# Optimization experiments

Measured on AMD Instinct MI355X. Metric: run time of the kernel, lower is better.

The kernel has to match this reference:

```python
import jax, jax.numpy as jnp
import numpy as np

DIM = 512
NUM_HEADS = 8
HEAD_DIM = DIM // NUM_HEADS
EPS = 1e-12  # F.normalize eps


def _l2norm(x):
    # F.normalize(x, dim=-1): x / max(||x||, eps)
    n = jnp.sqrt(jnp.sum(x * x, axis=-1, keepdims=True))
    return x / jnp.maximum(n, EPS)


def setup_inputs() -> dict:
    key = jax.random.key(0)
    ks = jax.random.split(key, 5)
    B, T, D = 4, 2048, DIM
    z = jax.random.normal(ks[0], (B, T, D), dtype=jnp.float32)
    t = jnp.zeros((1,), dtype=jnp.float32)  # unused ODE time
    omega = jax.random.normal(ks[1], (1, 1, D), dtype=jnp.float32) * 0.1
    # nn.Linear default init scale ~ U(-1/sqrt(fan_in), 1/sqrt(fan_in))
    s = 1.0 / np.sqrt(D)
    W_qk = jax.random.uniform(ks[2], (2 * D, D), jnp.float32, -s, s)
    W_out = jax.random.uniform(ks[3], (D, D), jnp.float32, -s, s)
    b_out = jax.random.uniform(ks[4], (D,), jnp.float32, -s, s)
    return {"t": t, "z": z, "omega": omega, "W_qk": W_qk, "W_out": W_out, "b_out": b_out}


def reference(t, z, omega, W_qk, W_out, b_out):
    B, T, D = z.shape
    H, hd = NUM_HEADS, HEAD_DIM
    qk = z @ W_qk.T                      # [B,T,2D]
    q, k = qk[..., :D], qk[..., D:]
    q = _l2norm(q.reshape(B, T, H, hd))  # [B,T,H,hd]
    k = _l2norm(k.reshape(B, T, H, hd))
    # coupling: [B,H,T,T]
    coupling = jnp.einsum("bqhd,bkhd->bhqk", q, k)
    interaction = jnp.sin(coupling)
    force = jnp.einsum("bhqk,bkhd->bqhd", interaction, k).reshape(B, T, D)
    return omega + force @ W_out.T + b_out
```

## Files before the change

### kernel.cpp

```cpp
#include <hip/hip_runtime.h>
#include <hip/hip_bf16.h>

typedef unsigned short u16;
typedef __attribute__((ext_vector_type(8))) short short8;
typedef __attribute__((ext_vector_type(4))) short short4_;
typedef __attribute__((ext_vector_type(4))) float f32x4;

#define B_ 4
#define T_ 2048
#define D_ 512
#define H_ 8
#define M_ (B_*T_)
#define INV2PI 0.15915494309189535f

__device__ u16   g_qb[M_*D_];
__device__ u16   g_kb[M_*D_];
__device__ u16   g_kTp[(size_t)B_*H_*64*T_];
__device__ float g_fA[(size_t)M_*D_];
__device__ float g_fB[(size_t)M_*D_];

__device__ inline u16 f2bf(float f) {
  union { __hip_bfloat16 h; u16 u; } cv;
  cv.h = __float2bfloat16(f);
  return cv.u;
}

__device__ inline float sin2pi(float x) {
#if __has_builtin(__builtin_amdgcn_sinf)
  return __builtin_amdgcn_sinf(x);
#else
  return __sinf(x * 6.283185307179586f);
#endif
}

__device__ inline short8 cvt8(f32x4 a, f32x4 b) {
  short8 o;
  o[0]=(short)f2bf(a[0]); o[1]=(short)f2bf(a[1]); o[2]=(short)f2bf(a[2]); o[3]=(short)f2bf(a[3]);
  o[4]=(short)f2bf(b[0]); o[5]=(short)f2bf(b[1]); o[6]=(short)f2bf(b[2]); o[7]=(short)f2bf(b[3]);
  return o;
}

__device__ inline int perm5(int p) {
  int lg = p >> 3, e = p & 7;
  return (e < 4) ? lg*4 + e : 16 + lg*4 + (e & 3);
}

template<int MODE>
__global__ __launch_bounds__(256, 2)
void gemm_bt(float* __restrict__ Cout, const float* __restrict__ add1,
             const float* __restrict__ add2, const float* __restrict__ Afp,
             const float* __restrict__ Bfp) {
  constexpr int K = 512;
  constexpr int N = (MODE == 0) ? 1024 : 512;
  __shared__ u16 As[128*72];
  __shared__ u16 Bs[128*72];
  const int m0 = blockIdx.x*128, n0 = blockIdx.y*128;
  const int t = threadIdx.x;
  const int w = t>>6, l = t&63;
  const int wr = (w>>1)*64, wc = (w&1)*64;
  const int lg = l>>4, li = l&15;
  const int srow = t>>3, scol = (t&7)*8;

  f32x4 acc[4][4] = {};

  for (int k0 = 0; k0 < K; k0 += 64) {
#pragma unroll
    for (int p = 0; p < 4; ++p) {
      int r = srow + p*32;
      {
        f32x4 b0 = *(const f32x4*)&Bfp[(size_t)(n0+r)*K + k0 + scol];
        f32x4 b1 = *(const f32x4*)&Bfp[(size_t)(n0+r)*K + k0 + scol + 4];
        *(short8*)&Bs[r*72 + scol] = cvt8(b0, b1);
      }
      if (MODE == 0) {
        f32x4 a0 = *(const f32x4*)&Afp[(size_t)(m0+r)*K + k0 + scol];
        f32x4 a1 = *(const f32x4*)&Afp[(size_t)(m0+r)*K + k0 + scol + 4];
        *(short8*)&As[r*72 + scol] = cvt8(a0, a1);
      } else {
        size_t off = (size_t)(m0+r)*K + k0 + scol;
        f32x4 a0 = *(const f32x4*)&g_fA[off];
        f32x4 a1 = *(const f32x4*)&g_fA[off+4];
        f32x4 c0 = *(const f32x4*)&g_fB[off];
        f32x4 c1 = *(const f32x4*)&g_fB[off+4];
        a0 += c0; a1 += c1;
        *(short8*)&As[r*72 + scol] = cvt8(a0, a1);
      }
    }
    __syncthreads();
#pragma unroll
    for (int ks = 0; ks < 2; ++ks) {
      short8 af[4], bf[4];
#pragma unroll
      for (int i = 0; i < 4; ++i)
        af[i] = *(const short8*)&As[(wr + i*16 + li)*72 + ks*32 + lg*8];
#pragma unroll
      for (int j = 0; j < 4; ++j)
        bf[j] = *(const short8*)&Bs[(wc + j*16 + li)*72 + ks*32 + lg*8];
#pragma unroll
      for (int i = 0; i < 4; ++i)
#pragma unroll
        for (int j = 0; j < 4; ++j)
          acc[i][j] = __builtin_amdgcn_mfma_f32_16x16x32_bf16(af[i], bf[j], acc[i][j], 0, 0, 0);
    }
    __syncthreads();
  }

  if (MODE == 0) {
    const bool isq = (n0 < 512);
    u16* dst = isq ? g_qb : g_kb;
    const float qs = isq ? INV2PI : 1.0f;
    const int nb = (isq ? n0 : n0 - 512) + wc;
#pragma unroll
    for (int i = 0; i < 4; ++i) {
#pragma unroll
      for (int r = 0; r < 4; ++r) {
        float s = 0.f;
#pragma unroll
        for (int j = 0; j < 4; ++j) s += acc[i][j][r]*acc[i][j][r];
#pragma unroll
        for (int off = 1; off < 16; off <<= 1) s += __shfl_xor(s, off);
        float sc = qs / fmaxf(sqrtf(s), 1e-12f);
        int row = m0 + wr + i*16 + lg*4 + r;
#pragma unroll
        for (int j = 0; j < 4; ++j)
          dst[(size_t)row*D_ + nb + j*16 + li] = f2bf(acc[i][j][r]*sc);
      }
    }
  } else {
#pragma unroll
    for (int i = 0; i < 4; ++i) {
#pragma unroll
      for (int j = 0; j < 4; ++j) {
        int col = n0 + wc + j*16 + li;
        float badd = add1[col] + add2[col];
#pragma unroll
        for (int r = 0; r < 4; ++r) {
          int row = m0 + wr + i*16 + lg*4 + r;
          Cout[(size_t)row*N + col] = acc[i][j][r] + badd;
        }
      }
    }
  }
}

__global__ void transpose_k_kernel() {
  __shared__ u16 tile[64*72];
  const int t0 = blockIdx.x*64, bh = blockIdx.y;
  const int b = bh>>3, h = bh&7;
  const int t = threadIdx.x;
  {
    int r = t>>2, cs = (t&3)*16;
    const u16* src = g_kb + (size_t)(b*T_ + t0 + r)*D_ + h*64 + cs;
    *(short8*)&tile[r*72 + cs]     = *(const short8*)(src);
    *(short8*)&tile[r*72 + cs + 8] = *(const short8*)(src + 8);
  }
  __syncthreads();
  {
    int d = t>>2, ts = (t&3)*16;
    short8 o0, o1;
#pragma unroll
    for (int j = 0; j < 8; ++j) {
      int p0 = ts + j, p1 = ts + 8 + j;
      int s0 = (p0 & ~31) | perm5(p0 & 31);
      int s1 = (p1 & ~31) | perm5(p1 & 31);
      o0[j] = (short)tile[s0*72 + d];
      o1[j] = (short)tile[s1*72 + d];
    }
    u16* dst = g_kTp + ((size_t)bh*64 + d)*T_ + t0 + ts;
    *(short8*)(dst)     = o0;
    *(short8*)(dst + 8) = o1;
  }
}

__global__ __launch_bounds__(256, 2)
void kuramoto_attn_kernel() {
  __shared__ u16 Ks[2][128*72];
  __shared__ u16 KTs[2][64*136];
  const int wg  = blockIdx.x;
  const int wgp = (wg & 7)*64 + (wg >> 3);
  const int bh = wgp >> 4, qt = (wgp & 15) >> 1, kh = wgp & 1;
  const int b = bh >> 3, h = bh & 7;
  const int t = threadIdx.x;
  const int w = t>>6, l = t&63;
  const int lg = l>>4, li = l&15;

  short8 bq[2][4];
#pragma unroll
  for (int ks = 0; ks < 2; ++ks)
#pragma unroll
    for (int j = 0; j < 4; ++j)
      bq[ks][j] = *(const short8*)&g_qb[(size_t)(b*T_ + qt*256 + w*64 + j*16 + li)*D_
                                        + h*64 + ks*32 + lg*8];

  const int sr = t>>3, sc = (t&7)*8;
  const int sd = t>>4, sk = (t&15)*8;
  const u16* kbase = g_kb  + (size_t)b*T_*D_ + h*64;
  const u16* tbase = g_kTp + (size_t)bh*64*T_;
  const int kt0 = kh*8;

  f32x4 acc_o[4][4] = {};

#pragma unroll
  for (int p = 0; p < 4; ++p) {
    *(short8*)&Ks[0][(sr + p*32)*72 + sc] =
      *(const short8*)&kbase[(size_t)(kt0*128 + sr + p*32)*D_ + sc];
    *(short8*)&KTs[0][(sd + p*16)*136 + sk] =
      *(const short8*)&tbase[(size_t)(sd + p*16)*T_ + kt0*128 + sk];
  }
  __syncthreads();

#pragma unroll 2
  for (int ii = 0; ii < 8; ++ii) {
    const int buf = ii & 1;
    short8 rk[4], rt[4];
    if (ii < 7) {
      const int ktn = kt0 + ii + 1;
#pragma unroll
      for (int p = 0; p < 4; ++p) {
        rk[p] = *(const short8*)&kbase[(size_t)(ktn*128 + sr + p*32)*D_ + sc];
        rt[p] = *(const short8*)&tbase[(size_t)(sd + p*16)*T_ + ktn*128 + sk];
      }
    }

#pragma unroll
    for (int kkp = 0; kkp < 4; ++kkp) {
      f32x4 sacc[2][4] = {};
#pragma unroll
      for (int ks = 0; ks < 2; ++ks) {
        short8 af0 = *(const short8*)&Ks[buf][((2*kkp  )*16 + li)*72 + ks*32 + lg*8];
        short8 af1 = *(const short8*)&Ks[buf][((2*kkp+1)*16 + li)*72 + ks*32 + lg*8];
#pragma unroll
        for (int j = 0; j < 4; ++j) {
          sacc[0][j] = __builtin_amdgcn_mfma_f32_16x16x32_bf16(af0, bq[ks][j], sacc[0][j], 0,0,0);
          sacc[1][j] = __builtin_amdgcn_mfma_f32_16x16x32_bf16(af1, bq[ks][j], sacc[1][j], 0,0,0);
        }
      }
      short8 apv[4];
#pragma unroll
      for (int j = 0; j < 4; ++j) {
        union { unsigned int u[4]; short8 s; } cv;
        cv.u[0] = (unsigned)f2bf(sin2pi(sacc[0][j][0])) | ((unsigned)f2bf(sin2pi(sacc[0][j][1]))<<16);
        cv.u[1] = (unsigned)f2bf(sin2pi(sacc[0][j][2])) | ((unsigned)f2bf(sin2pi(sacc[0][j][3]))<<16);
        cv.u[2] = (unsigned)f2bf(sin2pi(sacc[1][j][0])) | ((unsigned)f2bf(sin2pi(sacc[1][j][1]))<<16);
        cv.u[3] = (unsigned)f2bf(sin2pi(sacc[1][j][2])) | ((unsigned)f2bf(sin2pi(sacc[1][j][3]))<<16);
        apv[j] = cv.s;
      }
#pragma unroll
      for (int di = 0; di < 4; ++di) {
        short8 bv = *(const short8*)&KTs[buf][(di*16 + li)*136 + kkp*32 + lg*8];
#pragma unroll
        for (int j = 0; j < 4; ++j)
          acc_o[j][di] = __builtin_amdgcn_mfma_f32_16x16x32_bf16(apv[j], bv, acc_o[j][di], 0,0,0);
      }
    }

    if (ii < 7) {
#pragma unroll
      for (int p = 0; p < 4; ++p) {
        *(short8*)&Ks[buf^1][(sr + p*32)*72 + sc] = rk[p];
        *(short8*)&KTs[buf^1][(sd + p*16)*136 + sk] = rt[p];
      }
    }
    __syncthreads();
  }

  float* F = kh ? g_fB : g_fA;
#pragma unroll
  for (int j = 0; j < 4; ++j)
#pragma unroll
    for (int di = 0; di < 4; ++di)
#pragma unroll
      for (int r = 0; r < 4; ++r) {
        int row = b*T_ + qt*256 + w*64 + j*16 + lg*4 + r;
        int col = h*64 + di*16 + li;
        F[(size_t)row*D_ + col] = acc_o[j][di][r];
      }
}

extern "C" void kernel_launch(void* const* d_in, const int* in_sizes, int n_in,
                              void* d_out, int out_size, void* d_ws, size_t ws_size,
                              hipStream_t stream) {
  const float* z     = (const float*)d_in[1];
  const float* omega = (const float*)d_in[2];
  const float* Wqk   = (const float*)d_in[3];
  const float* Wout  = (const float*)d_in[4];
  const float* bout  = (const float*)d_in[5];
  float* out = (float*)d_out;

  gemm_bt<0><<<dim3(M_/128, 1024/128), 256, 0, stream>>>(nullptr, nullptr, nullptr, z, Wqk);
  transpose_k_kernel<<<dim3(T_/64, B_*H_), 256, 0, stream>>>();
  kuramoto_attn_kernel<<<512, 256, 0, stream>>>();
  gemm_bt<1><<<dim3(M_/128, 512/128), 256, 0, stream>>>(out, omega, bout, nullptr, Wout);
}
```

Before: 160.1 us.

## Switch to fp16 MFMA, drop key-split partials, software-pipeline QK and sin-PV

All matrix operands move from bf16 to fp16 with packed round-toward-zero conversions. The attention kernel no longer splits keys across two workgroups, so it launches 256 blocks that each loop over all 16 key tiles and write one fp16 force buffer. That buffer is read directly by the output GEMM, which removes the two fp32 partial buffers and their summation. The QK MFMAs for the next sub-tile are interleaved with the sin and PV stage of the previous one to overlap transcendental work with matrix work. This halves the grid to 256 blocks on a GPU with more compute units than that, which risks leaving some units idle, and the pipelining raises register pressure.

```diff
diff --git a/kernel.cpp b/kernel.cpp
--- a/kernel.cpp
+++ b/kernel.cpp
@@ -2,8 +2,10 @@
 #include <hip/hip_bf16.h>
 
 typedef unsigned short u16;
+typedef _Float16 f16;
+typedef __attribute__((ext_vector_type(8))) _Float16 f16x8;
+typedef __attribute__((ext_vector_type(2))) __fp16 h16x2;
 typedef __attribute__((ext_vector_type(8))) short short8;
-typedef __attribute__((ext_vector_type(4))) short short4_;
 typedef __attribute__((ext_vector_type(4))) float f32x4;
 
 #define B_ 4
@@ -13,17 +15,10 @@
 #define M_ (B_*T_)
 #define INV2PI 0.15915494309189535f
 
-__device__ u16   g_qb[M_*D_];
-__device__ u16   g_kb[M_*D_];
-__device__ u16   g_kTp[(size_t)B_*H_*64*T_];
-__device__ float g_fA[(size_t)M_*D_];
-__device__ float g_fB[(size_t)M_*D_];
-
-__device__ inline u16 f2bf(float f) {
-  union { __hip_bfloat16 h; u16 u; } cv;
-  cv.h = __float2bfloat16(f);
-  return cv.u;
-}
+__device__ f16 g_qb[M_*D_];
+__device__ f16 g_kb[M_*D_];
+__device__ f16 g_kTp[(size_t)B_*H_*64*T_];
+__device__ f16 g_force[(size_t)M_*D_];
 
 __device__ inline float sin2pi(float x) {
 #if __has_builtin(__builtin_amdgcn_sinf)
@@ -33,11 +28,13 @@
 #endif
 }
 
-__device__ inline short8 cvt8(f32x4 a, f32x4 b) {
-  short8 o;
-  o[0]=(short)f2bf(a[0]); o[1]=(short)f2bf(a[1]); o[2]=(short)f2bf(a[2]); o[3]=(short)f2bf(a[3]);
-  o[4]=(short)f2bf(b[0]); o[5]=(short)f2bf(b[1]); o[6]=(short)f2bf(b[2]); o[7]=(short)f2bf(b[3]);
-  return o;
+__device__ inline f16x8 cvt8h(f32x4 a, f32x4 b) {
+  union { h16x2 h[4]; f16x8 v; } u;
+  u.h[0] = __builtin_amdgcn_cvt_pkrtz(a[0], a[1]);
+  u.h[1] = __builtin_amdgcn_cvt_pkrtz(a[2], a[3]);
+  u.h[2] = __builtin_amdgcn_cvt_pkrtz(b[0], b[1]);
+  u.h[3] = __builtin_amdgcn_cvt_pkrtz(b[2], b[3]);
+  return u.v;
 }
 
 __device__ inline int perm5(int p) {
@@ -52,8 +49,8 @@
              const float* __restrict__ Bfp) {
   constexpr int K = 512;
   constexpr int N = (MODE == 0) ? 1024 : 512;
-  __shared__ u16 As[128*72];
-  __shared__ u16 Bs[128*72];
+  __shared__ f16 As[128*72];
+  __shared__ f16 Bs[128*72];
   const int m0 = blockIdx.x*128, n0 = blockIdx.y*128;
   const int t = threadIdx.x;
   const int w = t>>6, l = t&63;
@@ -70,44 +67,39 @@
       {
         f32x4 b0 = *(const f32x4*)&Bfp[(size_t)(n0+r)*K + k0 + scol];
         f32x4 b1 = *(const f32x4*)&Bfp[(size_t)(n0+r)*K + k0 + scol + 4];
-        *(short8*)&Bs[r*72 + scol] = cvt8(b0, b1);
+        *(f16x8*)&Bs[r*72 + scol] = cvt8h(b0, b1);
       }
       if (MODE == 0) {
         f32x4 a0 = *(const f32x4*)&Afp[(size_t)(m0+r)*K + k0 + scol];
         f32x4 a1 = *(const f32x4*)&Afp[(size_t)(m0+r)*K + k0 + scol + 4];
-        *(short8*)&As[r*72 + scol] = cvt8(a0, a1);
+        *(f16x8*)&As[r*72 + scol] = cvt8h(a0, a1);
       } else {
-        size_t off = (size_t)(m0+r)*K + k0 + scol;
-        f32x4 a0 = *(const f32x4*)&g_fA[off];
-        f32x4 a1 = *(const f32x4*)&g_fA[off+4];
-        f32x4 c0 = *(const f32x4*)&g_fB[off];
-        f32x4 c1 = *(const f32x4*)&g_fB[off+4];
-        a0 += c0; a1 += c1;
-        *(short8*)&As[r*72 + scol] = cvt8(a0, a1);
+        *(short8*)&As[r*72 + scol] =
+          *(const short8*)&g_force[(size_t)(m0+r)*K + k0 + scol];
       }
     }
     __syncthreads();
 #pragma unroll
     for (int ks = 0; ks < 2; ++ks) {
-      short8 af[4], bf[4];
+      f16x8 af[4], bf[4];
 #pragma unroll
       for (int i = 0; i < 4; ++i)
-        af[i] = *(const short8*)&As[(wr + i*16 + li)*72 + ks*32 + lg*8];
+        af[i] = *(const f16x8*)&As[(wr + i*16 + li)*72 + ks*32 + lg*8];
 #pragma unroll
       for (int j = 0; j < 4; ++j)
-        bf[j] = *(const short8*)&Bs[(wc + j*16 + li)*72 + ks*32 + lg*8];
+        bf[j] = *(const f16x8*)&Bs[(wc + j*16 + li)*72 + ks*32 + lg*8];
 #pragma unroll
       for (int i = 0; i < 4; ++i)
 #pragma unroll
         for (int j = 0; j < 4; ++j)
-          acc[i][j] = __builtin_amdgcn_mfma_f32_16x16x32_bf16(af[i], bf[j], acc[i][j], 0, 0, 0);
+          acc[i][j] = __builtin_amdgcn_mfma_f32_16x16x32_f16(af[i], bf[j], acc[i][j], 0, 0, 0);
     }
     __syncthreads();
   }
 
   if (MODE == 0) {
     const bool isq = (n0 < 512);
-    u16* dst = isq ? g_qb : g_kb;
+    f16* dst = isq ? g_qb : g_kb;
     const float qs = isq ? INV2PI : 1.0f;
     const int nb = (isq ? n0 : n0 - 512) + wc;
 #pragma unroll
@@ -123,7 +115,7 @@
         int row = m0 + wr + i*16 + lg*4 + r;
 #pragma unroll
         for (int j = 0; j < 4; ++j)
-          dst[(size_t)row*D_ + nb + j*16 + li] = f2bf(acc[i][j][r]*sc);
+          dst[(size_t)row*D_ + nb + j*16 + li] = (f16)(acc[i][j][r]*sc);
       }
     }
   } else {
@@ -148,9 +140,11 @@
   const int t0 = blockIdx.x*64, bh = blockIdx.y;
   const int b = bh>>3, h = bh&7;
   const int t = threadIdx.x;
+  const u16* kb = (const u16*)g_kb;
+  u16* kT = (u16*)g_kTp;
   {
     int r = t>>2, cs = (t&3)*16;
-    const u16* src = g_kb + (size_t)(b*T_ + t0 + r)*D_ + h*64 + cs;
+    const u16* src = kb + (size_t)(b*T_ + t0 + r)*D_ + h*64 + cs;
     *(short8*)&tile[r*72 + cs]     = *(const short8*)(src);
     *(short8*)&tile[r*72 + cs + 8] = *(const short8*)(src + 8);
   }
@@ -166,55 +160,78 @@
       o0[j] = (short)tile[s0*72 + d];
       o1[j] = (short)tile[s1*72 + d];
     }
-    u16* dst = g_kTp + ((size_t)bh*64 + d)*T_ + t0 + ts;
+    u16* dst = kT + ((size_t)bh*64 + d)*T_ + t0 + ts;
     *(short8*)(dst)     = o0;
     *(short8*)(dst + 8) = o1;
   }
 }
 
-__global__ __launch_bounds__(256, 2)
+__global__ __launch_bounds__(256)
 void kuramoto_attn_kernel() {
   __shared__ u16 Ks[2][128*72];
   __shared__ u16 KTs[2][64*136];
   const int wg  = blockIdx.x;
-  const int wgp = (wg & 7)*64 + (wg >> 3);
-  const int bh = wgp >> 4, qt = (wgp & 15) >> 1, kh = wgp & 1;
+  const int wgp = (wg & 7)*32 + (wg >> 3);
+  const int bh = wgp >> 3, qt = wgp & 7;
   const int b = bh >> 3, h = bh & 7;
   const int t = threadIdx.x;
   const int w = t>>6, l = t&63;
   const int lg = l>>4, li = l&15;
 
-  short8 bq[2][4];
+  f16x8 bq[2][4];
 #pragma unroll
   for (int ks = 0; ks < 2; ++ks)
 #pragma unroll
     for (int j = 0; j < 4; ++j)
-      bq[ks][j] = *(const short8*)&g_qb[(size_t)(b*T_ + qt*256 + w*64 + j*16 + li)*D_
-                                        + h*64 + ks*32 + lg*8];
+      bq[ks][j] = *(const f16x8*)&g_qb[(size_t)(b*T_ + qt*256 + w*64 + j*16 + li)*D_
+                                       + h*64 + ks*32 + lg*8];
 
   const int sr = t>>3, sc = (t&7)*8;
   const int sd = t>>4, sk = (t&15)*8;
-  const u16* kbase = g_kb  + (size_t)b*T_*D_ + h*64;
-  const u16* tbase = g_kTp + (size_t)bh*64*T_;
-  const int kt0 = kh*8;
+  const u16* kbase = (const u16*)g_kb  + (size_t)b*T_*D_ + h*64;
+  const u16* tbase = (const u16*)g_kTp + (size_t)bh*64*T_;
 
   f32x4 acc_o[4][4] = {};
 
 #pragma unroll
   for (int p = 0; p < 4; ++p) {
     *(short8*)&Ks[0][(sr + p*32)*72 + sc] =
-      *(const short8*)&kbase[(size_t)(kt0*128 + sr + p*32)*D_ + sc];
+      *(const short8*)&kbase[(size_t)(sr + p*32)*D_ + sc];
     *(short8*)&KTs[0][(sd + p*16)*136 + sk] =
-      *(const short8*)&tbase[(size_t)(sd + p*16)*T_ + kt0*128 + sk];
+      *(const short8*)&tbase[(size_t)(sd + p*16)*T_ + sk];
   }
   __syncthreads();
 
+#define QK_STEP(KKP, S) do {                                                   \
+  _Pragma("unroll") for (int ks = 0; ks < 2; ++ks) {                           \
+    f16x8 af0 = *(const f16x8*)&Ks[buf][((2*(KKP)  )*16 + li)*72 + ks*32 + lg*8]; \
+    f16x8 af1 = *(const f16x8*)&Ks[buf][((2*(KKP)+1)*16 + li)*72 + ks*32 + lg*8]; \
+    _Pragma("unroll") for (int j = 0; j < 4; ++j) {                            \
+      S[0][j] = __builtin_amdgcn_mfma_f32_16x16x32_f16(af0, bq[ks][j], S[0][j], 0,0,0); \
+      S[1][j] = __builtin_amdgcn_mfma_f32_16x16x32_f16(af1, bq[ks][j], S[1][j], 0,0,0); \
+    } } } while(0)
+
+#define SINPV_STEP(KKP, S) do {                                                \
+  f16x8 apv[4];                                                                \
+  _Pragma("unroll") for (int j = 0; j < 4; ++j) {                              \
+    union { h16x2 h[4]; f16x8 v; } cv;                                         \
+    cv.h[0] = __builtin_amdgcn_cvt_pkrtz(sin2pi(S[0][j][0]), sin2pi(S[0][j][1])); \
+    cv.h[1] = __builtin_amdgcn_cvt_pkrtz(sin2pi(S[0][j][2]), sin2pi(S[0][j][3])); \
+    cv.h[2] = __builtin_amdgcn_cvt_pkrtz(sin2pi(S[1][j][0]), sin2pi(S[1][j][1])); \
+    cv.h[3] = __builtin_amdgcn_cvt_pkrtz(sin2pi(S[1][j][2]), sin2pi(S[1][j][3])); \
+    apv[j] = cv.v; }                                                           \
+  _Pragma("unroll") for (int di = 0; di < 4; ++di) {                           \
+    f16x8 bv = *(const f16x8*)&KTs[buf][(di*16 + li)*136 + (KKP)*32 + lg*8];   \
+    _Pragma("unroll") for (int j = 0; j < 4; ++j)                              \
+      acc_o[j][di] = __builtin_amdgcn_mfma_f32_16x16x32_f16(apv[j], bv, acc_o[j][di], 0,0,0); \
+  } } while(0)
+
 #pragma unroll 2
-  for (int ii = 0; ii < 8; ++ii) {
+  for (int ii = 0; ii < 16; ++ii) {
     const int buf = ii & 1;
     short8 rk[4], rt[4];
-    if (ii < 7) {
-      const int ktn = kt0 + ii + 1;
+    if (ii < 15) {
+      const int ktn = ii + 1;
 #pragma unroll
       for (int p = 0; p < 4; ++p) {
         rk[p] = *(const short8*)&kbase[(size_t)(ktn*128 + sr + p*32)*D_ + sc];
@@ -222,39 +239,23 @@
       }
     }
 
-#pragma unroll
-    for (int kkp = 0; kkp < 4; ++kkp) {
-      f32x4 sacc[2][4] = {};
-#pragma unroll
-      for (int ks = 0; ks < 2; ++ks) {
-        short8 af0 = *(const short8*)&Ks[buf][((2*kkp  )*16 + li)*72 + ks*32 + lg*8];
-        short8 af1 = *(const short8*)&Ks[buf][((2*kkp+1)*16 + li)*72 + ks*32 + lg*8];
-#pragma unroll
-        for (int j = 0; j < 4; ++j) {
-          sacc[0][j] = __builtin_amdgcn_mfma_f32_16x16x32_bf16(af0, bq[ks][j], sacc[0][j], 0,0,0);
-          sacc[1][j] = __builtin_amdgcn_mfma_f32_16x16x32_bf16(af1, bq[ks][j], sacc[1][j], 0,0,0);
-        }
-      }
-      short8 apv[4];
-#pragma unroll
-      for (int j = 0; j < 4; ++j) {
-        union { unsigned int u[4]; short8 s; } cv;
-        cv.u[0] = (unsigned)f2bf(sin2pi(sacc[0][j][0])) | ((unsigned)f2bf(sin2pi(sacc[0][j][1]))<<16);
-        cv.u[1] = (unsigned)f2bf(sin2pi(sacc[0][j][2])) | ((unsigned)f2bf(sin2pi(sacc[0][j][3]))<<16);
-        cv.u[2] = (unsigned)f2bf(sin2pi(sacc[1][j][0])) | ((unsigned)f2bf(sin2pi(sacc[1][j][1]))<<16);
-        cv.u[3] = (unsigned)f2bf(sin2pi(sacc[1][j][2])) | ((unsigned)f2bf(sin2pi(sacc[1][j][3]))<<16);
-        apv[j] = cv.s;
-      }
-#pragma unroll
-      for (int di = 0; di < 4; ++di) {
-        short8 bv = *(const short8*)&KTs[buf][(di*16 + li)*136 + kkp*32 + lg*8];
-#pragma unroll
-        for (int j = 0; j < 4; ++j)
-          acc_o[j][di] = __builtin_amdgcn_mfma_f32_16x16x32_bf16(apv[j], bv, acc_o[j][di], 0,0,0);
-      }
-    }
-
-    if (ii < 7) {
+    f32x4 sA[2][4] = {};
+    f32x4 sB[2][4] = {};
+    QK_STEP(0, sA);
+    QK_STEP(1, sB);  SINPV_STEP(0, sA);
+#pragma unroll
+    for (int z = 0; z < 2; ++z)
+#pragma unroll
+      for (int j = 0; j < 4; ++j) sA[z][j] = (f32x4)(0.f);
+    QK_STEP(2, sA);  SINPV_STEP(1, sB);
+#pragma unroll
+    for (int z = 0; z < 2; ++z)
+#pragma unroll
+      for (int j = 0; j < 4; ++j) sB[z][j] = (f32x4)(0.f);
+    QK_STEP(3, sB);  SINPV_STEP(2, sA);
+                     SINPV_STEP(3, sB);
+
+    if (ii < 15) {
 #pragma unroll
       for (int p = 0; p < 4; ++p) {
         *(short8*)&Ks[buf^1][(sr + p*32)*72 + sc] = rk[p];
@@ -263,8 +264,9 @@
     }
     __syncthreads();
   }
-
-  float* F = kh ? g_fB : g_fA;
+#undef QK_STEP
+#undef SINPV_STEP
+
 #pragma unroll
   for (int j = 0; j < 4; ++j)
 #pragma unroll
@@ -273,7 +275,7 @@
       for (int r = 0; r < 4; ++r) {
         int row = b*T_ + qt*256 + w*64 + j*16 + lg*4 + r;
         int col = h*64 + di*16 + li;
-        F[(size_t)row*D_ + col] = acc_o[j][di][r];
+        g_force[(size_t)row*D_ + col] = (f16)acc_o[j][di][r];
       }
 }
 
@@ -289,6 +291,6 @@
 
   gemm_bt<0><<<dim3(M_/128, 1024/128), 256, 0, stream>>>(nullptr, nullptr, nullptr, z, Wqk);
   transpose_k_kernel<<<dim3(T_/64, B_*H_), 256, 0, stream>>>();
-  kuramoto_attn_kernel<<<512, 256, 0, stream>>>();
+  kuramoto_attn_kernel<<<256, 256, 0, stream>>>();
   gemm_bt<1><<<dim3(M_/128, 512/128), 256, 0, stream>>>(out, omega, bout, nullptr, Wout);
 }
```

New measurement: 155.3 us. 1.03x faster.
